# Kernel tuning notes

Measured on AMD Instinct MI355X. Metric: run time of the kernel, lower is better.

## Reference

```python
import jax, jax.numpy as jnp
import numpy as np

B = 64          # batch == number of parallel fc layers used
T = 512         # sequence length
IN_FEATS = 1024
OUT_FEATS = 1024


def setup_inputs() -> dict:
    key = jax.random.key(0)
    kx, kw, kb = jax.random.split(key, 3)
    x = jax.random.normal(kx, (B, T, IN_FEATS), dtype=jnp.float32)
    # Per-sample Linear weights, stacked: W[i] is the weight of list_fc[i]
    # (torch Linear weight layout: [out_feats, in_feats])
    bound = 1.0 / np.sqrt(IN_FEATS)
    W = jax.random.uniform(kw, (B, OUT_FEATS, IN_FEATS), dtype=jnp.float32,
                           minval=-bound, maxval=bound)
    b = jax.random.uniform(kb, (B, OUT_FEATS), dtype=jnp.float32,
                           minval=-bound, maxval=bound)
    return {"x": x, "W": W, "b": b}


def reference(x, W, b):
    # Equivalent to: cat([list_fc[i](x[i:i+1]) for i in range(B)], dim=0)
    # i.e. a grouped GEMM with group size 1: out[i] = x[i] @ W[i].T + b[i]
    out = jnp.einsum('bti,boi->bto', x, W)  # [B, T, OUT]
    return out + b[:, None, :]
```

## Files before the change

kernel.cpp:

```cpp
#include <hip/hip_runtime.h>
#include <hip/hip_bf16.h>

#define BATCH 64
#define MDIM 512
#define NDIM 1024
#define KDIM 1024

#define BM 256
#define BN 256
#define BK 64
#define NKT (KDIM / BK)

typedef __attribute__((ext_vector_type(4))) float f32x4;
typedef __attribute__((ext_vector_type(8))) short bf16x8;
typedef __attribute__((ext_vector_type(4))) unsigned int u32x4;

__device__ __forceinline__ unsigned int cvt2(float lo, float hi) {
    __hip_bfloat162 h = __float22bfloat162_rn(float2{lo, hi});
    return *(unsigned int*)&h;
}

#define MFMA16(a, b, c) __builtin_amdgcn_mfma_f32_16x16x32_bf16((a), (b), (c), 0, 0, 0)
#define SB0 __builtin_amdgcn_sched_barrier(0)
#define WAITLG(n) do { asm volatile("s_waitcnt lgkmcnt(" #n ")" ::: "memory"); SB0; } while (0)
#define BAR do { SB0; __builtin_amdgcn_s_barrier(); SB0; } while (0)

__global__ __launch_bounds__(512, 2)
void grouped_fc_kernel(const float* __restrict__ X,
                       const float* __restrict__ W,
                       const float* __restrict__ Bias,
                       float* __restrict__ Out) {
    const int swz  = (blockIdx.x & 7) * 64 + (blockIdx.x >> 3);
    const int bidx = swz >> 3;
    const int tile = swz & 7;
    const int tm = tile & 1;
    const int tn = tile >> 1;

    const int tid  = threadIdx.x;
    const int lane = tid & 63;
    const int wid  = tid >> 6;
    const int wm   = wid & 1;
    const int wn   = wid >> 1;

    __shared__ unsigned short ldsA[2][BM][BK];
    __shared__ unsigned short ldsB[2][BN][BK];

    const float* srcA = X + ((size_t)bidx * MDIM + (size_t)tm * BM) * KDIM;
    const float* srcB = W + ((size_t)bidx * NDIM + (size_t)tn * BN) * KDIM;

    const int s_r  = tid >> 2;
    const int s_cf = (tid & 3) * 16;
    const int s_x  = s_r & 7;
    const int so0  = (((tid & 3) * 2)     ^ s_x) * 8;
    const int so1  = (((tid & 3) * 2 + 1) ^ s_x) * 8;

    f32x4 st0[4], st1[4];

    auto ISSUE = [&](const float* srcbase, int hv, int kt_, f32x4 (&s)[4]) {
        const float* p = srcbase + (size_t)(hv * 128 + s_r) * KDIM + kt_ * BK + s_cf;
#pragma unroll
        for (int v = 0; v < 4; ++v) s[v] = *(const f32x4*)(p + v * 4);
    };

    auto CVTW = [&](unsigned short* ldsbase, int hv, f32x4 (&s)[4]) {
        const int row = hv * 128 + s_r;
        u32x4 w0, w1;
        w0[0] = cvt2(s[0][0], s[0][1]); w0[1] = cvt2(s[0][2], s[0][3]);
        w0[2] = cvt2(s[1][0], s[1][1]); w0[3] = cvt2(s[1][2], s[1][3]);
        w1[0] = cvt2(s[2][0], s[2][1]); w1[1] = cvt2(s[2][2], s[2][3]);
        w1[2] = cvt2(s[3][0], s[3][1]); w1[3] = cvt2(s[3][2], s[3][3]);
        *(u32x4*)&ldsbase[(size_t)row * BK + so0] = w0;
        *(u32x4*)&ldsbase[(size_t)row * BK + so1] = w1;
    };

    const int frow = lane & 15;
    const int khi  = lane >> 4;
    const int xr   = frow & 7;
    const int oK0  = ((khi)     ^ xr) * 8;
    const int oK1  = ((4 + khi) ^ xr) * 8;

    auto rdA = [&](int buf, int mi, int o) {
        return *(const bf16x8*)&ldsA[buf][wm * 128 + mi * 16 + frow][o];
    };
    auto rdB = [&](int buf, int ni, int o) {
        return *(const bf16x8*)&ldsB[buf][wn * 64 + ni * 16 + frow][o];
    };

    f32x4 acc[8][4];
#pragma unroll
    for (int mi = 0; mi < 8; ++mi)
#pragma unroll
        for (int ni = 0; ni < 4; ++ni)
            acc[mi][ni] = (f32x4){0.f, 0.f, 0.f, 0.f};

    ISSUE(srcA, 0, 0, st0); ISSUE(srcA, 1, 0, st1);
    CVTW(&ldsA[0][0][0], 0, st0); CVTW(&ldsA[0][0][0], 1, st1);
    ISSUE(srcB, 0, 0, st0); ISSUE(srcB, 1, 0, st1);
    CVTW(&ldsB[0][0][0], 0, st0); CVTW(&ldsB[0][0][0], 1, st1);
    ISSUE(srcA, 0, 1, st0); ISSUE(srcA, 1, 1, st1);
    WAITLG(0);
    BAR;

    bf16x8 af[8], bfr[4];

#pragma unroll 1
    for (int kt = 0; kt < NKT - 1; ++kt) {
        const int rd = kt & 1;
        const bool m2 = (kt + 2 < NKT);
        unsigned short* nA = &ldsA[rd ^ 1][0][0];
        unsigned short* nB = &ldsB[rd ^ 1][0][0];

#pragma unroll
        for (int mi = 0; mi < 8; ++mi) af[mi] = rdA(rd, mi, oK0);
        bfr[0] = rdB(rd, 0, oK0); bfr[1] = rdB(rd, 1, oK0);
        WAITLG(0);
        __builtin_amdgcn_s_setprio(1);
#pragma unroll
        for (int mi = 0; mi < 8; ++mi) {
            acc[mi][0] = MFMA16(af[mi], bfr[0], acc[mi][0]);
            acc[mi][1] = MFMA16(af[mi], bfr[1], acc[mi][1]);
        }
        __builtin_amdgcn_s_setprio(0);
        bfr[2] = rdB(rd, 2, oK0); bfr[3] = rdB(rd, 3, oK0);
        SB0;
        CVTW(nA, 0, st0);
        ISSUE(srcB, 0, kt + 1, st0);
        BAR;

        WAITLG(2);
        __builtin_amdgcn_s_setprio(1);
#pragma unroll
        for (int mi = 0; mi < 8; ++mi) {
            acc[mi][2] = MFMA16(af[mi], bfr[2], acc[mi][2]);
            acc[mi][3] = MFMA16(af[mi], bfr[3], acc[mi][3]);
        }
        __builtin_amdgcn_s_setprio(0);
#pragma unroll
        for (int mi = 0; mi < 8; ++mi) af[mi] = rdA(rd, mi, oK1);
        bfr[0] = rdB(rd, 0, oK1); bfr[1] = rdB(rd, 1, oK1);
        SB0;
        CVTW(nA, 1, st1);
        ISSUE(srcB, 1, kt + 1, st1);
        BAR;

        WAITLG(2);
        __builtin_amdgcn_s_setprio(1);
#pragma unroll
        for (int mi = 0; mi < 8; ++mi) {
            acc[mi][0] = MFMA16(af[mi], bfr[0], acc[mi][0]);
            acc[mi][1] = MFMA16(af[mi], bfr[1], acc[mi][1]);
        }
        __builtin_amdgcn_s_setprio(0);
        bfr[2] = rdB(rd, 2, oK1); bfr[3] = rdB(rd, 3, oK1);
        SB0;
        CVTW(nB, 0, st0); CVTW(nB, 1, st1);
        if (m2) ISSUE(srcA, 0, kt + 2, st0);
        BAR;

        WAITLG(4);
        __builtin_amdgcn_s_setprio(1);
#pragma unroll
        for (int mi = 0; mi < 8; ++mi) {
            acc[mi][2] = MFMA16(af[mi], bfr[2], acc[mi][2]);
            acc[mi][3] = MFMA16(af[mi], bfr[3], acc[mi][3]);
        }
        __builtin_amdgcn_s_setprio(0);
        if (m2) ISSUE(srcA, 1, kt + 2, st1);
        WAITLG(0);
        BAR;
    }

    {
        const int rd = (NKT - 1) & 1;
#pragma unroll
        for (int mi = 0; mi < 8; ++mi) af[mi] = rdA(rd, mi, oK0);
#pragma unroll
        for (int ni = 0; ni < 4; ++ni) bfr[ni] = rdB(rd, ni, oK0);
        WAITLG(0);
#pragma unroll
        for (int mi = 0; mi < 8; ++mi)
#pragma unroll
            for (int ni = 0; ni < 4; ++ni)
                acc[mi][ni] = MFMA16(af[mi], bfr[ni], acc[mi][ni]);
#pragma unroll
        for (int mi = 0; mi < 8; ++mi) af[mi] = rdA(rd, mi, oK1);
#pragma unroll
        for (int ni = 0; ni < 4; ++ni) bfr[ni] = rdB(rd, ni, oK1);
        WAITLG(0);
#pragma unroll
        for (int mi = 0; mi < 8; ++mi)
#pragma unroll
            for (int ni = 0; ni < 4; ++ni)
                acc[mi][ni] = MFMA16(af[mi], bfr[ni], acc[mi][ni]);
    }

#pragma unroll
    for (int ni = 0; ni < 4; ++ni) {
        const int gc = tn * BN + wn * 64 + ni * 16 + frow;
        const float bv = Bias[bidx * NDIM + gc];
#pragma unroll
        for (int mi = 0; mi < 8; ++mi) {
            const int gr0 = tm * BM + wm * 128 + mi * 16 + khi * 4;
            float* po = Out + ((size_t)bidx * MDIM + gr0) * NDIM + gc;
#pragma unroll
            for (int r = 0; r < 4; ++r)
                po[(size_t)r * NDIM] = acc[mi][ni][r] + bv;
        }
    }
}

extern "C" void kernel_launch(void* const* d_in, const int* in_sizes, int n_in,
                              void* d_out, int out_size, void* d_ws, size_t ws_size,
                              hipStream_t stream) {
    const float* X  = (const float*)d_in[0];
    const float* W  = (const float*)d_in[1];
    const float* Bs = (const float*)d_in[2];
    float* Out = (float*)d_out;

    grouped_fc_kernel<<<dim3(512), dim3(512), 0, stream>>>(X, W, Bs, Out);
}
```

Before: 137.5 us.

## Double workgroup to 1024 threads with 64x64 warp tiles and simpler staging

The workgroup grows from 8 to 16 waves over the same 256x256 output tile, so each wave now computes a 64x64 sub-tile instead of 128x64. Each thread stages one row segment of A and one of B per K-step instead of two, and the pipelined K loop is rebuilt so one phase no longer carries conversion or load work. The goal is more resident waves to hide global and LDS latency, with lower per-thread register pressure. The cost is more LDS fragment reads per MFMA and a launch bound that may constrain register allocation.

```diff
diff --git a/kernel.cpp b/kernel.cpp
--- a/kernel.cpp
+++ b/kernel.cpp
@@ -25,7 +25,7 @@
 #define WAITLG(n) do { asm volatile("s_waitcnt lgkmcnt(" #n ")" ::: "memory"); SB0; } while (0)
 #define BAR do { SB0; __builtin_amdgcn_s_barrier(); SB0; } while (0)
 
-__global__ __launch_bounds__(512, 2)
+__global__ __launch_bounds__(1024, 4)
 void grouped_fc_kernel(const float* __restrict__ X,
                        const float* __restrict__ W,
                        const float* __restrict__ Bias,
@@ -39,8 +39,8 @@
     const int tid  = threadIdx.x;
     const int lane = tid & 63;
     const int wid  = tid >> 6;
-    const int wm   = wid & 1;
-    const int wn   = wid >> 1;
+    const int wm   = wid & 3;
+    const int wn   = wid >> 2;
 
     __shared__ unsigned short ldsA[2][BM][BK];
     __shared__ unsigned short ldsB[2][BN][BK];
@@ -54,23 +54,22 @@
     const int so0  = (((tid & 3) * 2)     ^ s_x) * 8;
     const int so1  = (((tid & 3) * 2 + 1) ^ s_x) * 8;
 
-    f32x4 st0[4], st1[4];
-
-    auto ISSUE = [&](const float* srcbase, int hv, int kt_, f32x4 (&s)[4]) {
-        const float* p = srcbase + (size_t)(hv * 128 + s_r) * KDIM + kt_ * BK + s_cf;
+    f32x4 stA[4], stB[4];
+
+    auto ISSUE = [&](const float* srcbase, int kt_, f32x4 (&s)[4]) {
+        const float* p = srcbase + (size_t)s_r * KDIM + kt_ * BK + s_cf;
 #pragma unroll
         for (int v = 0; v < 4; ++v) s[v] = *(const f32x4*)(p + v * 4);
     };
 
-    auto CVTW = [&](unsigned short* ldsbase, int hv, f32x4 (&s)[4]) {
-        const int row = hv * 128 + s_r;
+    auto CVTW = [&](unsigned short* ldsbase, f32x4 (&s)[4]) {
         u32x4 w0, w1;
         w0[0] = cvt2(s[0][0], s[0][1]); w0[1] = cvt2(s[0][2], s[0][3]);
         w0[2] = cvt2(s[1][0], s[1][1]); w0[3] = cvt2(s[1][2], s[1][3]);
         w1[0] = cvt2(s[2][0], s[2][1]); w1[1] = cvt2(s[2][2], s[2][3]);
         w1[2] = cvt2(s[3][0], s[3][1]); w1[3] = cvt2(s[3][2], s[3][3]);
-        *(u32x4*)&ldsbase[(size_t)row * BK + so0] = w0;
-        *(u32x4*)&ldsbase[(size_t)row * BK + so1] = w1;
+        *(u32x4*)&ldsbase[(size_t)s_r * BK + so0] = w0;
+        *(u32x4*)&ldsbase[(size_t)s_r * BK + so1] = w1;
     };
 
     const int frow = lane & 15;
@@ -80,28 +79,26 @@
     const int oK1  = ((4 + khi) ^ xr) * 8;
 
     auto rdA = [&](int buf, int mi, int o) {
-        return *(const bf16x8*)&ldsA[buf][wm * 128 + mi * 16 + frow][o];
+        return *(const bf16x8*)&ldsA[buf][wm * 64 + mi * 16 + frow][o];
     };
     auto rdB = [&](int buf, int ni, int o) {
         return *(const bf16x8*)&ldsB[buf][wn * 64 + ni * 16 + frow][o];
     };
 
-    f32x4 acc[8][4];
-#pragma unroll
-    for (int mi = 0; mi < 8; ++mi)
+    f32x4 acc[4][4];
+#pragma unroll
+    for (int mi = 0; mi < 4; ++mi)
 #pragma unroll
         for (int ni = 0; ni < 4; ++ni)
             acc[mi][ni] = (f32x4){0.f, 0.f, 0.f, 0.f};
 
-    ISSUE(srcA, 0, 0, st0); ISSUE(srcA, 1, 0, st1);
-    CVTW(&ldsA[0][0][0], 0, st0); CVTW(&ldsA[0][0][0], 1, st1);
-    ISSUE(srcB, 0, 0, st0); ISSUE(srcB, 1, 0, st1);
-    CVTW(&ldsB[0][0][0], 0, st0); CVTW(&ldsB[0][0][0], 1, st1);
-    ISSUE(srcA, 0, 1, st0); ISSUE(srcA, 1, 1, st1);
+    ISSUE(srcA, 0, stA); CVTW(&ldsA[0][0][0], stA);
+    ISSUE(srcB, 0, stB); CVTW(&ldsB[0][0][0], stB);
+    ISSUE(srcA, 1, stA);
     WAITLG(0);
     BAR;
 
-    bf16x8 af[8], bfr[4];
+    bf16x8 af[4], bfr[4];
 
 #pragma unroll 1
     for (int kt = 0; kt < NKT - 1; ++kt) {
@@ -111,61 +108,57 @@
         unsigned short* nB = &ldsB[rd ^ 1][0][0];
 
 #pragma unroll
-        for (int mi = 0; mi < 8; ++mi) af[mi] = rdA(rd, mi, oK0);
+        for (int mi = 0; mi < 4; ++mi) af[mi] = rdA(rd, mi, oK0);
         bfr[0] = rdB(rd, 0, oK0); bfr[1] = rdB(rd, 1, oK0);
         WAITLG(0);
         __builtin_amdgcn_s_setprio(1);
 #pragma unroll
-        for (int mi = 0; mi < 8; ++mi) {
+        for (int mi = 0; mi < 4; ++mi) {
             acc[mi][0] = MFMA16(af[mi], bfr[0], acc[mi][0]);
             acc[mi][1] = MFMA16(af[mi], bfr[1], acc[mi][1]);
         }
         __builtin_amdgcn_s_setprio(0);
         bfr[2] = rdB(rd, 2, oK0); bfr[3] = rdB(rd, 3, oK0);
         SB0;
-        CVTW(nA, 0, st0);
-        ISSUE(srcB, 0, kt + 1, st0);
+        CVTW(nA, stA);
+        ISSUE(srcB, kt + 1, stB);
         BAR;
 
         WAITLG(2);
         __builtin_amdgcn_s_setprio(1);
 #pragma unroll
-        for (int mi = 0; mi < 8; ++mi) {
+        for (int mi = 0; mi < 4; ++mi) {
             acc[mi][2] = MFMA16(af[mi], bfr[2], acc[mi][2]);
             acc[mi][3] = MFMA16(af[mi], bfr[3], acc[mi][3]);
         }
         __builtin_amdgcn_s_setprio(0);
 #pragma unroll
-        for (int mi = 0; mi < 8; ++mi) af[mi] = rdA(rd, mi, oK1);
+        for (int mi = 0; mi < 4; ++mi) af[mi] = rdA(rd, mi, oK1);
         bfr[0] = rdB(rd, 0, oK1); bfr[1] = rdB(rd, 1, oK1);
-        SB0;
-        CVTW(nA, 1, st1);
-        ISSUE(srcB, 1, kt + 1, st1);
-        BAR;
-
-        WAITLG(2);
-        __builtin_amdgcn_s_setprio(1);
-#pragma unroll
-        for (int mi = 0; mi < 8; ++mi) {
+        BAR;
+
+        WAITLG(0);
+        __builtin_amdgcn_s_setprio(1);
+#pragma unroll
+        for (int mi = 0; mi < 4; ++mi) {
             acc[mi][0] = MFMA16(af[mi], bfr[0], acc[mi][0]);
             acc[mi][1] = MFMA16(af[mi], bfr[1], acc[mi][1]);
         }
         __builtin_amdgcn_s_setprio(0);
         bfr[2] = rdB(rd, 2, oK1); bfr[3] = rdB(rd, 3, oK1);
         SB0;
-        CVTW(nB, 0, st0); CVTW(nB, 1, st1);
-        if (m2) ISSUE(srcA, 0, kt + 2, st0);
-        BAR;
-
-        WAITLG(4);
-        __builtin_amdgcn_s_setprio(1);
-#pragma unroll
-        for (int mi = 0; mi < 8; ++mi) {
+        CVTW(nB, stB);
+        if (m2) ISSUE(srcA, kt + 2, stA);
+        BAR;
+
+        WAITLG(2);
+        __builtin_amdgcn_s_setprio(1);
+#pragma unroll
+        for (int mi = 0; mi < 4; ++mi) {
             acc[mi][2] = MFMA16(af[mi], bfr[2], acc[mi][2]);
             acc[mi][3] = MFMA16(af[mi], bfr[3], acc[mi][3]);
         }
         __builtin_amdgcn_s_setprio(0);
-        if (m2) ISSUE(srcA, 1, kt + 2, st1);
         WAITLG(0);
         BAR;
     }
@@ -173,22 +166,22 @@
     {
         const int rd = (NKT - 1) & 1;
 #pragma unroll
-        for (int mi = 0; mi < 8; ++mi) af[mi] = rdA(rd, mi, oK0);
+        for (int mi = 0; mi < 4; ++mi) af[mi] = rdA(rd, mi, oK0);
 #pragma unroll
         for (int ni = 0; ni < 4; ++ni) bfr[ni] = rdB(rd, ni, oK0);
         WAITLG(0);
 #pragma unroll
-        for (int mi = 0; mi < 8; ++mi)
+        for (int mi = 0; mi < 4; ++mi)
 #pragma unroll
             for (int ni = 0; ni < 4; ++ni)
                 acc[mi][ni] = MFMA16(af[mi], bfr[ni], acc[mi][ni]);
 #pragma unroll
-        for (int mi = 0; mi < 8; ++mi) af[mi] = rdA(rd, mi, oK1);
+        for (int mi = 0; mi < 4; ++mi) af[mi] = rdA(rd, mi, oK1);
 #pragma unroll
         for (int ni = 0; ni < 4; ++ni) bfr[ni] = rdB(rd, ni, oK1);
         WAITLG(0);
 #pragma unroll
-        for (int mi = 0; mi < 8; ++mi)
+        for (int mi = 0; mi < 4; ++mi)
 #pragma unroll
             for (int ni = 0; ni < 4; ++ni)
                 acc[mi][ni] = MFMA16(af[mi], bfr[ni], acc[mi][ni]);
@@ -199,8 +192,8 @@
         const int gc = tn * BN + wn * 64 + ni * 16 + frow;
         const float bv = Bias[bidx * NDIM + gc];
 #pragma unroll
-        for (int mi = 0; mi < 8; ++mi) {
-            const int gr0 = tm * BM + wm * 128 + mi * 16 + khi * 4;
+        for (int mi = 0; mi < 4; ++mi) {
+            const int gr0 = tm * BM + wm * 64 + mi * 16 + khi * 4;
             float* po = Out + ((size_t)bidx * MDIM + gr0) * NDIM + gc;
 #pragma unroll
             for (int r = 0; r < 4; ++r)
@@ -217,5 +210,5 @@
     const float* Bs = (const float*)d_in[2];
     float* Out = (float*)d_out;
 
-    grouped_fc_kernel<<<dim3(512), dim3(512), 0, stream>>>(X, W, Bs, Out);
+    grouped_fc_kernel<<<dim3(512), dim3(1024), 0, stream>>>(X, W, Bs, Out);
 }
```

After: 188.8 us. +37.3%, slower.

## Process both M tiles per block with cross-tile prefetch, halving the grid

Applied to the files above, without the earlier changes.

Each block now computes both 256-row M tiles for its batch and N tile in sequence, so the launch shrinks from 512 to 256 blocks. The loads and LDS writes for the second tile's first K step are issued during the tail of the first tile, so its prologue overlaps the first tile's last MFMAs and the store of its results. The aim is to remove the second scheduling wave and the exposed per-block prologue and epilogue, given that LDS use limits residency to about one block per CU. The W tile is still re-streamed from global memory for the second M tile, and each block now runs twice as long.

```diff
diff --git a/kernel.cpp b/kernel.cpp
--- a/kernel.cpp
+++ b/kernel.cpp
@@ -30,11 +30,9 @@
                        const float* __restrict__ W,
                        const float* __restrict__ Bias,
                        float* __restrict__ Out) {
-    const int swz  = (blockIdx.x & 7) * 64 + (blockIdx.x >> 3);
-    const int bidx = swz >> 3;
-    const int tile = swz & 7;
-    const int tm = tile & 1;
-    const int tn = tile >> 1;
+    const int swz  = (blockIdx.x & 7) * 32 + (blockIdx.x >> 3);
+    const int bidx = swz >> 2;
+    const int tn   = swz & 3;
 
     const int tid  = threadIdx.x;
     const int lane = tid & 63;
@@ -45,8 +43,9 @@
     __shared__ unsigned short ldsA[2][BM][BK];
     __shared__ unsigned short ldsB[2][BN][BK];
 
-    const float* srcA = X + ((size_t)bidx * MDIM + (size_t)tm * BM) * KDIM;
-    const float* srcB = W + ((size_t)bidx * NDIM + (size_t)tn * BN) * KDIM;
+    const float* srcA0 = X + ((size_t)bidx * MDIM + 0 * BM) * KDIM;
+    const float* srcA1 = X + ((size_t)bidx * MDIM + 1 * BM) * KDIM;
+    const float* srcB  = W + ((size_t)bidx * NDIM + (size_t)tn * BN) * KDIM;
 
     const int s_r  = tid >> 2;
     const int s_cf = (tid & 3) * 16;
@@ -93,118 +92,153 @@
         for (int ni = 0; ni < 4; ++ni)
             acc[mi][ni] = (f32x4){0.f, 0.f, 0.f, 0.f};
 
-    ISSUE(srcA, 0, 0, st0); ISSUE(srcA, 1, 0, st1);
+    ISSUE(srcA0, 0, 0, st0); ISSUE(srcA0, 1, 0, st1);
     CVTW(&ldsA[0][0][0], 0, st0); CVTW(&ldsA[0][0][0], 1, st1);
     ISSUE(srcB, 0, 0, st0); ISSUE(srcB, 1, 0, st1);
     CVTW(&ldsB[0][0][0], 0, st0); CVTW(&ldsB[0][0][0], 1, st1);
-    ISSUE(srcA, 0, 1, st0); ISSUE(srcA, 1, 1, st1);
+    ISSUE(srcA0, 0, 1, st0); ISSUE(srcA0, 1, 1, st1);
     WAITLG(0);
     BAR;
 
     bf16x8 af[8], bfr[4];
 
+#pragma unroll
+    for (int tm = 0; tm < 2; ++tm) {
+        const float* srcA = tm ? srcA1 : srcA0;
+
 #pragma unroll 1
-    for (int kt = 0; kt < NKT - 1; ++kt) {
-        const int rd = kt & 1;
-        const bool m2 = (kt + 2 < NKT);
-        unsigned short* nA = &ldsA[rd ^ 1][0][0];
-        unsigned short* nB = &ldsB[rd ^ 1][0][0];
-
-#pragma unroll
-        for (int mi = 0; mi < 8; ++mi) af[mi] = rdA(rd, mi, oK0);
-        bfr[0] = rdB(rd, 0, oK0); bfr[1] = rdB(rd, 1, oK0);
-        WAITLG(0);
-        __builtin_amdgcn_s_setprio(1);
-#pragma unroll
-        for (int mi = 0; mi < 8; ++mi) {
-            acc[mi][0] = MFMA16(af[mi], bfr[0], acc[mi][0]);
-            acc[mi][1] = MFMA16(af[mi], bfr[1], acc[mi][1]);
-        }
-        __builtin_amdgcn_s_setprio(0);
-        bfr[2] = rdB(rd, 2, oK0); bfr[3] = rdB(rd, 3, oK0);
-        SB0;
-        CVTW(nA, 0, st0);
-        ISSUE(srcB, 0, kt + 1, st0);
-        BAR;
-
-        WAITLG(2);
-        __builtin_amdgcn_s_setprio(1);
-#pragma unroll
-        for (int mi = 0; mi < 8; ++mi) {
-            acc[mi][2] = MFMA16(af[mi], bfr[2], acc[mi][2]);
-            acc[mi][3] = MFMA16(af[mi], bfr[3], acc[mi][3]);
-        }
-        __builtin_amdgcn_s_setprio(0);
-#pragma unroll
-        for (int mi = 0; mi < 8; ++mi) af[mi] = rdA(rd, mi, oK1);
-        bfr[0] = rdB(rd, 0, oK1); bfr[1] = rdB(rd, 1, oK1);
-        SB0;
-        CVTW(nA, 1, st1);
-        ISSUE(srcB, 1, kt + 1, st1);
-        BAR;
-
-        WAITLG(2);
-        __builtin_amdgcn_s_setprio(1);
-#pragma unroll
-        for (int mi = 0; mi < 8; ++mi) {
-            acc[mi][0] = MFMA16(af[mi], bfr[0], acc[mi][0]);
-            acc[mi][1] = MFMA16(af[mi], bfr[1], acc[mi][1]);
-        }
-        __builtin_amdgcn_s_setprio(0);
-        bfr[2] = rdB(rd, 2, oK1); bfr[3] = rdB(rd, 3, oK1);
-        SB0;
-        CVTW(nB, 0, st0); CVTW(nB, 1, st1);
-        if (m2) ISSUE(srcA, 0, kt + 2, st0);
-        BAR;
-
-        WAITLG(4);
-        __builtin_amdgcn_s_setprio(1);
-#pragma unroll
-        for (int mi = 0; mi < 8; ++mi) {
-            acc[mi][2] = MFMA16(af[mi], bfr[2], acc[mi][2]);
-            acc[mi][3] = MFMA16(af[mi], bfr[3], acc[mi][3]);
-        }
-        __builtin_amdgcn_s_setprio(0);
-        if (m2) ISSUE(srcA, 1, kt + 2, st1);
-        WAITLG(0);
-        BAR;
-    }
-
-    {
-        const int rd = (NKT - 1) & 1;
-#pragma unroll
-        for (int mi = 0; mi < 8; ++mi) af[mi] = rdA(rd, mi, oK0);
-#pragma unroll
-        for (int ni = 0; ni < 4; ++ni) bfr[ni] = rdB(rd, ni, oK0);
-        WAITLG(0);
-#pragma unroll
-        for (int mi = 0; mi < 8; ++mi)
-#pragma unroll
-            for (int ni = 0; ni < 4; ++ni)
-                acc[mi][ni] = MFMA16(af[mi], bfr[ni], acc[mi][ni]);
-#pragma unroll
-        for (int mi = 0; mi < 8; ++mi) af[mi] = rdA(rd, mi, oK1);
-#pragma unroll
-        for (int ni = 0; ni < 4; ++ni) bfr[ni] = rdB(rd, ni, oK1);
-        WAITLG(0);
-#pragma unroll
-        for (int mi = 0; mi < 8; ++mi)
-#pragma unroll
-            for (int ni = 0; ni < 4; ++ni)
-                acc[mi][ni] = MFMA16(af[mi], bfr[ni], acc[mi][ni]);
-    }
-
-#pragma unroll
-    for (int ni = 0; ni < 4; ++ni) {
-        const int gc = tn * BN + wn * 64 + ni * 16 + frow;
-        const float bv = Bias[bidx * NDIM + gc];
-#pragma unroll
-        for (int mi = 0; mi < 8; ++mi) {
-            const int gr0 = tm * BM + wm * 128 + mi * 16 + khi * 4;
-            float* po = Out + ((size_t)bidx * MDIM + gr0) * NDIM + gc;
-#pragma unroll
-            for (int r = 0; r < 4; ++r)
-                po[(size_t)r * NDIM] = acc[mi][ni][r] + bv;
+        for (int kt = 0; kt < NKT - 1; ++kt) {
+            const int rd = kt & 1;
+            const bool m2 = (kt + 2 < NKT);
+            unsigned short* nA = &ldsA[rd ^ 1][0][0];
+            unsigned short* nB = &ldsB[rd ^ 1][0][0];
+
+#pragma unroll
+            for (int mi = 0; mi < 8; ++mi) af[mi] = rdA(rd, mi, oK0);
+            bfr[0] = rdB(rd, 0, oK0); bfr[1] = rdB(rd, 1, oK0);
+            WAITLG(0);
+            __builtin_amdgcn_s_setprio(1);
+#pragma unroll
+            for (int mi = 0; mi < 8; ++mi) {
+                acc[mi][0] = MFMA16(af[mi], bfr[0], acc[mi][0]);
+                acc[mi][1] = MFMA16(af[mi], bfr[1], acc[mi][1]);
+            }
+            __builtin_amdgcn_s_setprio(0);
+            bfr[2] = rdB(rd, 2, oK0); bfr[3] = rdB(rd, 3, oK0);
+            SB0;
+            CVTW(nA, 0, st0);
+            ISSUE(srcB, 0, kt + 1, st0);
+            BAR;
+
+            WAITLG(2);
+            __builtin_amdgcn_s_setprio(1);
+#pragma unroll
+            for (int mi = 0; mi < 8; ++mi) {
+                acc[mi][2] = MFMA16(af[mi], bfr[2], acc[mi][2]);
+                acc[mi][3] = MFMA16(af[mi], bfr[3], acc[mi][3]);
+            }
+            __builtin_amdgcn_s_setprio(0);
+#pragma unroll
+            for (int mi = 0; mi < 8; ++mi) af[mi] = rdA(rd, mi, oK1);
+            bfr[0] = rdB(rd, 0, oK1); bfr[1] = rdB(rd, 1, oK1);
+            SB0;
+            CVTW(nA, 1, st1);
+            ISSUE(srcB, 1, kt + 1, st1);
+            BAR;
+
+            WAITLG(2);
+            __builtin_amdgcn_s_setprio(1);
+#pragma unroll
+            for (int mi = 0; mi < 8; ++mi) {
+                acc[mi][0] = MFMA16(af[mi], bfr[0], acc[mi][0]);
+                acc[mi][1] = MFMA16(af[mi], bfr[1], acc[mi][1]);
+            }
+            __builtin_amdgcn_s_setprio(0);
+            bfr[2] = rdB(rd, 2, oK1); bfr[3] = rdB(rd, 3, oK1);
+            SB0;
+            CVTW(nB, 0, st0); CVTW(nB, 1, st1);
+            if (m2)           ISSUE(srcA, 0, kt + 2, st0);
+            else if (tm == 0) ISSUE(srcA1, 0, 0, st0);
+            BAR;
+
+            WAITLG(4);
+            __builtin_amdgcn_s_setprio(1);
+#pragma unroll
+            for (int mi = 0; mi < 8; ++mi) {
+                acc[mi][2] = MFMA16(af[mi], bfr[2], acc[mi][2]);
+                acc[mi][3] = MFMA16(af[mi], bfr[3], acc[mi][3]);
+            }
+            __builtin_amdgcn_s_setprio(0);
+            if (m2)           ISSUE(srcA, 1, kt + 2, st1);
+            else if (tm == 0) ISSUE(srcA1, 1, 0, st1);
+            WAITLG(0);
+            BAR;
+        }
+
+        {
+            const int rd = (NKT - 1) & 1;
+#pragma unroll
+            for (int mi = 0; mi < 8; ++mi) af[mi] = rdA(rd, mi, oK0);
+#pragma unroll
+            for (int ni = 0; ni < 4; ++ni) bfr[ni] = rdB(rd, ni, oK0);
+            WAITLG(0);
+            __builtin_amdgcn_s_setprio(1);
+#pragma unroll
+            for (int mi = 0; mi < 8; ++mi)
+#pragma unroll
+                for (int ni = 0; ni < 4; ++ni)
+                    acc[mi][ni] = MFMA16(af[mi], bfr[ni], acc[mi][ni]);
+            __builtin_amdgcn_s_setprio(0);
+            SB0;
+#pragma unroll
+            for (int mi = 0; mi < 8; ++mi) af[mi] = rdA(rd, mi, oK1);
+#pragma unroll
+            for (int ni = 0; ni < 4; ++ni) bfr[ni] = rdB(rd, ni, oK1);
+            SB0;
+            if (tm == 0) {
+                CVTW(&ldsA[0][0][0], 0, st0);
+                CVTW(&ldsA[0][0][0], 1, st1);
+                WAITLG(4);
+            } else {
+                WAITLG(0);
+            }
+            __builtin_amdgcn_s_setprio(1);
+#pragma unroll
+            for (int mi = 0; mi < 8; ++mi)
+#pragma unroll
+                for (int ni = 0; ni < 4; ++ni)
+                    acc[mi][ni] = MFMA16(af[mi], bfr[ni], acc[mi][ni]);
+            __builtin_amdgcn_s_setprio(0);
+            if (tm == 0) {
+                ISSUE(srcB, 0, 0, st0); ISSUE(srcB, 1, 0, st1);
+                CVTW(&ldsB[0][0][0], 0, st0);
+                CVTW(&ldsB[0][0][0], 1, st1);
+            }
+        }
+
+#pragma unroll
+        for (int ni = 0; ni < 4; ++ni) {
+            const int gc = tn * BN + wn * 64 + ni * 16 + frow;
+            const float bv = Bias[bidx * NDIM + gc];
+#pragma unroll
+            for (int mi = 0; mi < 8; ++mi) {
+                const int gr0 = tm * BM + wm * 128 + mi * 16 + khi * 4;
+                float* po = Out + ((size_t)bidx * MDIM + gr0) * NDIM + gc;
+#pragma unroll
+                for (int r = 0; r < 4; ++r)
+                    po[(size_t)r * NDIM] = acc[mi][ni][r] + bv;
+            }
+        }
+
+        if (tm == 0) {
+#pragma unroll
+            for (int mi = 0; mi < 8; ++mi)
+#pragma unroll
+                for (int ni = 0; ni < 4; ++ni)
+                    acc[mi][ni] = (f32x4){0.f, 0.f, 0.f, 0.f};
+            ISSUE(srcA1, 0, 1, st0); ISSUE(srcA1, 1, 1, st1);
+            WAITLG(0);
+            BAR;
         }
     }
 }
@@ -217,5 +251,5 @@
     const float* Bs = (const float*)d_in[2];
     float* Out = (float*)d_out;
 
-    grouped_fc_kernel<<<dim3(512), dim3(512), 0, stream>>>(X, W, Bs, Out);
+    grouped_fc_kernel<<<dim3(256), dim3(512), 0, stream>>>(X, W, Bs, Out);
 }
```

After: 201.9 us. +46.9%, slower.
